# Kernel tuning notes

Measured on AMD Instinct MI355X. Metric: run time of the kernel, lower is better.

Reference implementation:

```python
import jax, jax.numpy as jnp
import numpy as np

N_NODES = 100000
N_EDGES = 1600000
G_DIM, H1, H2 = 128, 64, 32
HEADS = 4
NUM_REL = 3
NUM_CLASSES = 7


def setup_inputs() -> dict:
    key = jax.random.key(0)
    ks = jax.random.split(key, 16)
    s = 0.05
    inp = {
        "x": jax.random.normal(ks[0], (N_NODES, G_DIM), dtype=jnp.float32),
        "lengths": N_NODES,
        "edge_index": jax.random.randint(ks[1], (2, N_EDGES), 0, N_NODES),
        "edge_type": jax.random.randint(ks[2], (N_EDGES,), 0, NUM_REL),
        # RGCNConv params (root weight + per-relation weights + bias)
        "W_rel": jax.random.normal(ks[3], (NUM_REL, G_DIM, H1), dtype=jnp.float32) * s,
        "W_root": jax.random.normal(ks[4], (G_DIM, H1), dtype=jnp.float32) * s,
        "b_rgcn": jax.random.normal(ks[5], (H1,), dtype=jnp.float32) * s,
        # TransformerConv params (heads*H2 = 128 output, concat=True default)
        "Wq": jax.random.normal(ks[6], (H1, HEADS * H2), dtype=jnp.float32) * s,
        "bq": jax.random.normal(ks[7], (HEADS * H2,), dtype=jnp.float32) * s,
        "Wk": jax.random.normal(ks[8], (H1, HEADS * H2), dtype=jnp.float32) * s,
        "bk": jax.random.normal(ks[9], (HEADS * H2,), dtype=jnp.float32) * s,
        "Wv": jax.random.normal(ks[10], (H1, HEADS * H2), dtype=jnp.float32) * s,
        "bv": jax.random.normal(ks[11], (HEADS * H2,), dtype=jnp.float32) * s,
        "Wskip": jax.random.normal(ks[12], (H1, HEADS * H2), dtype=jnp.float32) * s,
        "bskip": jax.random.normal(ks[13], (HEADS * H2,), dtype=jnp.float32) * s,
        # final classifier (in = heads*H2 since TransformerConv concat=True)
        "Wf": jax.random.normal(ks[14], (HEADS * H2, NUM_CLASSES), dtype=jnp.float32) * s,
        "bf": jax.random.normal(ks[15], (NUM_CLASSES,), dtype=jnp.float32) * s,
    }
    return inp


def _forward(x, edge_index, edge_type, W_rel, W_root, b_rgcn,
             Wq, bq, Wk, bk, Wv, bv, Wskip, bskip, Wf, bf):
    n = x.shape[0]
    src, dst = edge_index[0], edge_index[1]  # source -> target flow

    # ---- RGCNConv: root transform + per-relation mean aggregation ----
    h = x @ W_root + b_rgcn  # [N, H1]
    for r in range(NUM_REL):
        hr = x @ W_rel[r]  # [N, H1] transform at node level (cheap)
        mask = (edge_type == r)
        msg = jnp.where(mask[:, None], hr[src], 0.0)  # [E, H1]
        ssum = jax.ops.segment_sum(msg, dst, num_segments=n)
        cnt = jax.ops.segment_sum(mask.astype(x.dtype), dst, num_segments=n)
        h = h + jnp.where(cnt[:, None] > 0, ssum / jnp.maximum(cnt, 1.0)[:, None], 0.0)
    h = jax.nn.relu(h)

    # ---- TransformerConv (heads=4, concat=True, root skip) ----
    Q = (h @ Wq + bq).reshape(n, HEADS, H2)
    K = (h @ Wk + bk).reshape(n, HEADS, H2)
    V = (h @ Wv + bv).reshape(n, HEADS, H2)
    scores = jnp.sum(Q[dst] * K[src], axis=-1) / jnp.sqrt(jnp.asarray(H2, x.dtype))  # [E, HEADS]
    smax = jax.ops.segment_max(scores, dst, num_segments=n)  # [N, HEADS]
    e = jnp.exp(scores - smax[dst])
    denom = jax.ops.segment_sum(e, dst, num_segments=n)  # [N, HEADS]
    alpha = e / jnp.maximum(denom[dst], 1e-16)  # [E, HEADS]
    agg = jax.ops.segment_sum(alpha[..., None] * V[src], dst, num_segments=n)  # [N, HEADS, H2]
    out = agg.reshape(n, HEADS * H2) + h @ Wskip + bskip
    out = jax.nn.relu(out)

    return out @ Wf + bf  # [N, NUM_CLASSES]


def reference(x, lengths, edge_index, edge_type, W_rel, W_root, b_rgcn,
              Wq, bq, Wk, bk, Wv, bv, Wskip, bskip, Wf, bf):
    # lengths is accepted but unused by the original forward
    return _forward(x, edge_index, edge_type, W_rel, W_root, b_rgcn,
                    Wq, bq, Wk, bk, Wv, bv, Wskip, bskip, Wf, bf)
```

## Files before the change

kernel.cpp:

```cpp
#include <hip/hip_runtime.h>
#include <math.h>

#define N_NODES 100000
#define N_EDGES 1600000

typedef short short8 __attribute__((ext_vector_type(8)));
typedef float f32x4 __attribute__((ext_vector_type(4)));

static __device__ __forceinline__ float bf2f(unsigned int u16) {
    return __uint_as_float(u16 << 16);
}
static __device__ __forceinline__ unsigned short f2bf(float f) {
    unsigned u = __float_as_uint(f);
    unsigned r = u + 0x7FFF + ((u >> 16) & 1);
    return (unsigned short)(r >> 16);
}

__global__ void repack_kernel(const float* __restrict__ Wrel, const float* __restrict__ Wroot,
                              const float* __restrict__ Wq, const float* __restrict__ Wk,
                              const float* __restrict__ Wv, const float* __restrict__ Wsk,
                              const float* __restrict__ bq, const float* __restrict__ bk,
                              const float* __restrict__ bv, const float* __restrict__ bsk,
                              unsigned short* __restrict__ W1t, unsigned short* __restrict__ W2t,
                              float* __restrict__ bcat) {
    int idx = blockIdx.x * 256 + threadIdx.x;
    if (idx < 128 * 256) {
        int k = idx >> 8, c = idx & 255;
        float v;
        if (c < 192) { int r = c >> 6, cc = c & 63; v = Wrel[r * 8192 + k * 64 + cc]; }
        else v = Wroot[k * 64 + (c - 192)];
        W1t[c * 128 + k] = f2bf(v);
    }
    int i2 = idx - 128 * 256;
    if (i2 >= 0 && i2 < 64 * 512) {
        int k = i2 >> 9, c = i2 & 511;
        float v;
        if (c < 128) v = Wq[k * 128 + c];
        else if (c < 256) v = Wk[k * 128 + c - 128];
        else if (c < 384) v = Wv[k * 128 + c - 256];
        else v = Wsk[k * 128 + c - 384];
        W2t[c * 64 + k] = f2bf(v);
    }
    int i3 = idx - 128 * 256 - 64 * 512;
    if (i3 >= 0 && i3 < 512) {
        float v;
        if (i3 < 128) v = bq[i3];
        else if (i3 < 256) v = bk[i3 - 128];
        else if (i3 < 384) v = bv[i3 - 256];
        else v = bsk[i3 - 384];
        bcat[i3] = v;
    }
}

__global__ void hist_kernel(const int* __restrict__ ei, int* __restrict__ deg) {
    int e = blockIdx.x * 256 + threadIdx.x;
    if (e < N_EDGES) atomicAdd(&deg[ei[N_EDGES + e]], 1);
}

__global__ void scanA_kernel(const int* __restrict__ deg, int* __restrict__ part) {
    __shared__ int wsum[4];
    int t = threadIdx.x;
    int base = blockIdx.x * 1024 + t * 4;
    int s = 0;
    for (int i = 0; i < 4; i++) { int idx = base + i; if (idx < N_NODES) s += deg[idx]; }
    for (int off = 1; off < 64; off <<= 1) s += __shfl_xor(s, off);
    if ((t & 63) == 0) wsum[t >> 6] = s;
    __syncthreads();
    if (t == 0) part[blockIdx.x] = wsum[0] + wsum[1] + wsum[2] + wsum[3];
}

__global__ void scanB_kernel(int* __restrict__ part, int* __restrict__ rs, int nb) {
    int run = 0;
    for (int b = 0; b < nb; b++) { int v = part[b]; part[b] = run; run += v; }
    rs[N_NODES] = run;
}

__global__ void scanC_kernel(const int* __restrict__ deg, const int* __restrict__ part,
                             int* __restrict__ rs) {
    __shared__ int wsum[4];
    int t = threadIdx.x;
    int base = blockIdx.x * 1024 + t * 4;
    int v[4]; int tsum = 0;
    for (int i = 0; i < 4; i++) { int idx = base + i; v[i] = (idx < N_NODES) ? deg[idx] : 0; tsum += v[i]; }
    int x = tsum;
    int lane = t & 63;
    for (int off = 1; off < 64; off <<= 1) { int y = __shfl_up(x, off); if (lane >= off) x += y; }
    if (lane == 63) wsum[t >> 6] = x;
    __syncthreads();
    if (t == 0) { int run = 0; for (int w = 0; w < 4; w++) { int tmp = wsum[w]; wsum[w] = run; run += tmp; } }
    __syncthreads();
    int excl = x - tsum + wsum[t >> 6] + part[blockIdx.x];
    for (int i = 0; i < 4; i++) {
        int idx = base + i;
        if (idx < N_NODES) rs[idx] = excl;
        excl += v[i];
    }
}

__global__ void scatter_kernel(const int* __restrict__ ei, const int* __restrict__ et,
                               const int* __restrict__ rs, int* __restrict__ fill,
                               unsigned int* __restrict__ ep) {
    int e = blockIdx.x * 256 + threadIdx.x;
    if (e >= N_EDGES) return;
    int src = ei[e], dst = ei[N_EDGES + e], r = et[e];
    int pos = rs[dst] + atomicAdd(&fill[dst], 1);
    ep[pos] = (unsigned)src | ((unsigned)r << 20);
}

__global__ __launch_bounds__(256) void gemm1_mfma(const float* __restrict__ X,
                                                  const unsigned short* __restrict__ W1t,
                                                  unsigned short* __restrict__ hr_all) {
    __shared__ unsigned short As[64][136];
    __shared__ unsigned short Bs[64][136];
    int t = threadIdx.x;
    int rb = blockIdx.x * 64;
    #pragma unroll
    for (int i = 0; i < 8; i++) {
        int lin = t + i * 256;
        int row = lin >> 5;
        int c4 = lin & 31;
        float4 v = make_float4(0.f, 0.f, 0.f, 0.f);
        int gr = rb + row;
        if (gr < N_NODES) v = *(const float4*)&X[gr * 128 + c4 * 4];
        unsigned w0 = (unsigned)f2bf(v.x) | ((unsigned)f2bf(v.y) << 16);
        unsigned w1 = (unsigned)f2bf(v.z) | ((unsigned)f2bf(v.w) << 16);
        *(uint2*)&As[row][c4 * 4] = make_uint2(w0, w1);
    }
    int w = t >> 6, l = t & 63;
    int wr = (w >> 1) * 32, wc = (w & 1) * 32;
    int lr = l & 15, lk = (l >> 4) * 8;
    int drow = (l >> 4) * 4;
    int dcol = l & 15;
    for (int cb4 = 0; cb4 < 4; cb4++) {
        int cb = cb4 * 64;
        __syncthreads();
        #pragma unroll
        for (int i = 0; i < 4; i++) {
            int lin = t + i * 256;
            int n = lin >> 4;
            int k8 = lin & 15;
            *(uint4*)&Bs[n][k8 * 8] = *(const uint4*)&W1t[(cb + n) * 128 + k8 * 8];
        }
        __syncthreads();
        f32x4 c00 = {0.f,0.f,0.f,0.f}, c01 = {0.f,0.f,0.f,0.f};
        f32x4 c10 = {0.f,0.f,0.f,0.f}, c11 = {0.f,0.f,0.f,0.f};
        #pragma unroll
        for (int kk = 0; kk < 128; kk += 32) {
            short8 a0 = *(const short8*)&As[wr + lr][kk + lk];
            short8 a1 = *(const short8*)&As[wr + 16 + lr][kk + lk];
            short8 b0 = *(const short8*)&Bs[wc + lr][kk + lk];
            short8 b1 = *(const short8*)&Bs[wc + 16 + lr][kk + lk];
            c00 = __builtin_amdgcn_mfma_f32_16x16x32_bf16(a0, b0, c00, 0, 0, 0);
            c01 = __builtin_amdgcn_mfma_f32_16x16x32_bf16(a0, b1, c01, 0, 0, 0);
            c10 = __builtin_amdgcn_mfma_f32_16x16x32_bf16(a1, b0, c10, 0, 0, 0);
            c11 = __builtin_amdgcn_mfma_f32_16x16x32_bf16(a1, b1, c11, 0, 0, 0);
        }
        f32x4 cc[2][2] = {{c00, c01}, {c10, c11}};
        #pragma unroll
        for (int i = 0; i < 2; i++)
            #pragma unroll
            for (int j = 0; j < 2; j++)
                #pragma unroll
                for (int rg = 0; rg < 4; rg++) {
                    int gr = rb + wr + i * 16 + drow + rg;
                    int gc = cb + wc + j * 16 + dcol;
                    if (gr < N_NODES) hr_all[gr * 256 + gc] = f2bf(cc[i][j][rg]);
                }
    }
}

__global__ __launch_bounds__(256) void rgcn_kernel(const unsigned short* __restrict__ hr,
                                                   const float* __restrict__ brg, const int* __restrict__ rs,
                                                   const unsigned int* __restrict__ ep,
                                                   unsigned short* __restrict__ Hm) {
    int lane = threadIdx.x & 63;
    int n = blockIdx.x * 4 + (threadIdx.x >> 6);
    if (n >= N_NODES) return;
    int p0 = rs[n], p1 = rs[n + 1];
    float a0 = 0.f, a1 = 0.f, a2 = 0.f, c0 = 0.f, c1 = 0.f, c2 = 0.f;
    for (int base = p0; base < p1; base += 64) {
        int pc = base + lane;
        int chunk = (pc < p1) ? (int)ep[pc] : 0;
        int cnt = min(64, p1 - base);
        int j = 0;
        for (; j + 3 < cnt; j += 4) {
            int e0 = __builtin_amdgcn_readlane(chunk, j);
            int e1 = __builtin_amdgcn_readlane(chunk, j + 1);
            int e2 = __builtin_amdgcn_readlane(chunk, j + 2);
            int e3 = __builtin_amdgcn_readlane(chunk, j + 3);
            int s0 = e0 & 0xFFFFF, r0 = e0 >> 20;
            int s1 = e1 & 0xFFFFF, r1 = e1 >> 20;
            int s2 = e2 & 0xFFFFF, r2 = e2 >> 20;
            int s3 = e3 & 0xFFFFF, r3 = e3 >> 20;
            float v0 = bf2f(hr[s0 * 256 + r0 * 64 + lane]);
            float v1 = bf2f(hr[s1 * 256 + r1 * 64 + lane]);
            float v2 = bf2f(hr[s2 * 256 + r2 * 64 + lane]);
            float v3 = bf2f(hr[s3 * 256 + r3 * 64 + lane]);
            if (r0 == 0) { a0 += v0; c0 += 1.f; } else if (r0 == 1) { a1 += v0; c1 += 1.f; } else { a2 += v0; c2 += 1.f; }
            if (r1 == 0) { a0 += v1; c0 += 1.f; } else if (r1 == 1) { a1 += v1; c1 += 1.f; } else { a2 += v1; c2 += 1.f; }
            if (r2 == 0) { a0 += v2; c0 += 1.f; } else if (r2 == 1) { a1 += v2; c1 += 1.f; } else { a2 += v2; c2 += 1.f; }
            if (r3 == 0) { a0 += v3; c0 += 1.f; } else if (r3 == 1) { a1 += v3; c1 += 1.f; } else { a2 += v3; c2 += 1.f; }
        }
        for (; j < cnt; j++) {
            int e0 = __builtin_amdgcn_readlane(chunk, j);
            int s0 = e0 & 0xFFFFF, r0 = e0 >> 20;
            float v0 = bf2f(hr[s0 * 256 + r0 * 64 + lane]);
            if (r0 == 0) { a0 += v0; c0 += 1.f; } else if (r0 == 1) { a1 += v0; c1 += 1.f; } else { a2 += v0; c2 += 1.f; }
        }
    }
    float h = bf2f(hr[n * 256 + 192 + lane]) + brg[lane];
    if (c0 > 0.f) h += a0 / c0;
    if (c1 > 0.f) h += a1 / c1;
    if (c2 > 0.f) h += a2 / c2;
    Hm[n * 64 + lane] = f2bf(fmaxf(h, 0.f));
}

__global__ __launch_bounds__(256) void gemm2_mfma(const unsigned short* __restrict__ Hm,
                                                  const unsigned short* __restrict__ W2t,
                                                  const float* __restrict__ bcat,
                                                  unsigned short* __restrict__ Qb, unsigned short* __restrict__ Kb,
                                                  unsigned short* __restrict__ Vb, unsigned short* __restrict__ Sb) {
    __shared__ unsigned short As[64][72];
    __shared__ unsigned short Bs[64][72];
    int t = threadIdx.x;
    int rb = blockIdx.x * 64;
    #pragma unroll
    for (int i = 0; i < 2; i++) {
        int lin = t + i * 256;
        int row = lin >> 3;
        int k8 = lin & 7;
        uint4 v = make_uint4(0, 0, 0, 0);
        int gr = rb + row;
        if (gr < N_NODES) v = *(const uint4*)&Hm[gr * 64 + k8 * 8];
        *(uint4*)&As[row][k8 * 8] = v;
    }
    int w = t >> 6, l = t & 63;
    int wr = (w >> 1) * 32, wc = (w & 1) * 32;
    int lr = l & 15, lk = (l >> 4) * 8;
    int drow = (l >> 4) * 4;
    int dcol = l & 15;
    for (int cb8 = 0; cb8 < 8; cb8++) {
        int cb = cb8 * 64;
        __syncthreads();
        #pragma unroll
        for (int i = 0; i < 2; i++) {
            int lin = t + i * 256;
            int n = lin >> 3;
            int k8 = lin & 7;
            *(uint4*)&Bs[n][k8 * 8] = *(const uint4*)&W2t[(cb + n) * 64 + k8 * 8];
        }
        __syncthreads();
        f32x4 c00 = {0.f,0.f,0.f,0.f}, c01 = {0.f,0.f,0.f,0.f};
        f32x4 c10 = {0.f,0.f,0.f,0.f}, c11 = {0.f,0.f,0.f,0.f};
        #pragma unroll
        for (int kk = 0; kk < 64; kk += 32) {
            short8 a0 = *(const short8*)&As[wr + lr][kk + lk];
            short8 a1 = *(const short8*)&As[wr + 16 + lr][kk + lk];
            short8 b0 = *(const short8*)&Bs[wc + lr][kk + lk];
            short8 b1 = *(const short8*)&Bs[wc + 16 + lr][kk + lk];
            c00 = __builtin_amdgcn_mfma_f32_16x16x32_bf16(a0, b0, c00, 0, 0, 0);
            c01 = __builtin_amdgcn_mfma_f32_16x16x32_bf16(a0, b1, c01, 0, 0, 0);
            c10 = __builtin_amdgcn_mfma_f32_16x16x32_bf16(a1, b0, c10, 0, 0, 0);
            c11 = __builtin_amdgcn_mfma_f32_16x16x32_bf16(a1, b1, c11, 0, 0, 0);
        }
        f32x4 cc[2][2] = {{c00, c01}, {c10, c11}};
        #pragma unroll
        for (int i = 0; i < 2; i++)
            #pragma unroll
            for (int j = 0; j < 2; j++)
                #pragma unroll
                for (int rg = 0; rg < 4; rg++) {
                    int gr = rb + wr + i * 16 + drow + rg;
                    int gc = cb + wc + j * 16 + dcol;
                    if (gr >= N_NODES) continue;
                    float v = cc[i][j][rg] + bcat[gc];
                    unsigned short h = f2bf(v);
                    if (gc < 128) Qb[gr * 128 + gc] = h;
                    else if (gc < 256) Kb[gr * 128 + (gc - 128)] = h;
                    else if (gc < 384) Vb[gr * 128 + (gc - 256)] = h;
                    else Sb[gr * 128 + (gc - 384)] = h;
                }
    }
}

__global__ __launch_bounds__(256) void attn_kernel(const unsigned short* __restrict__ Qb,
                                                   const unsigned short* __restrict__ Kb,
                                                   const unsigned short* __restrict__ Vb,
                                                   const int* __restrict__ rs, const unsigned int* __restrict__ ep,
                                                   const unsigned short* __restrict__ Sb,
                                                   const float* __restrict__ Wf, const float* __restrict__ bfv,
                                                   float* __restrict__ out) {
    int lane = threadIdx.x & 63;
    int n = blockIdx.x * 4 + (threadIdx.x >> 6);
    if (n >= N_NODES) return;
    const unsigned* Qu = (const unsigned*)Qb;
    const unsigned* Ku = (const unsigned*)Kb;
    const unsigned* Vu = (const unsigned*)Vb;
    const unsigned* Su = (const unsigned*)Sb;
    unsigned qw = Qu[n * 64 + lane];
    const float qs = 0.17677669529663687f;
    float q0 = bf2f(qw & 0xFFFF) * qs, q1 = bf2f(qw >> 16) * qs;
    float wf0[7], wf1[7];
    #pragma unroll
    for (int j = 0; j < 7; j++) { wf0[j] = Wf[(2 * lane) * 7 + j]; wf1[j] = Wf[(2 * lane + 1) * 7 + j]; }
    float d = 0.f, o0 = 0.f, o1 = 0.f;
    int p0 = rs[n], p1 = rs[n + 1];
    for (int base = p0; base < p1; base += 64) {
        int pc = base + lane;
        int chunk = (pc < p1) ? (int)ep[pc] : 0;
        int cnt = min(64, p1 - base);
        int j = 0;
        for (; j + 3 < cnt; j += 4) {
            int e0 = __builtin_amdgcn_readlane(chunk, j);
            int e1 = __builtin_amdgcn_readlane(chunk, j + 1);
            int e2 = __builtin_amdgcn_readlane(chunk, j + 2);
            int e3 = __builtin_amdgcn_readlane(chunk, j + 3);
            int s0 = e0 & 0xFFFFF, s1 = e1 & 0xFFFFF, s2 = e2 & 0xFFFFF, s3 = e3 & 0xFFFFF;
            unsigned k0 = Ku[s0 * 64 + lane], k1 = Ku[s1 * 64 + lane];
            unsigned k2 = Ku[s2 * 64 + lane], k3 = Ku[s3 * 64 + lane];
            unsigned v0 = Vu[s0 * 64 + lane], v1 = Vu[s1 * 64 + lane];
            unsigned v2 = Vu[s2 * 64 + lane], v3 = Vu[s3 * 64 + lane];
            float d0 = q0 * bf2f(k0 & 0xFFFF) + q1 * bf2f(k0 >> 16);
            float d1 = q0 * bf2f(k1 & 0xFFFF) + q1 * bf2f(k1 >> 16);
            float d2 = q0 * bf2f(k2 & 0xFFFF) + q1 * bf2f(k2 >> 16);
            float d3 = q0 * bf2f(k3 & 0xFFFF) + q1 * bf2f(k3 >> 16);
            d0 += __shfl_xor(d0, 1); d1 += __shfl_xor(d1, 1); d2 += __shfl_xor(d2, 1); d3 += __shfl_xor(d3, 1);
            d0 += __shfl_xor(d0, 2); d1 += __shfl_xor(d1, 2); d2 += __shfl_xor(d2, 2); d3 += __shfl_xor(d3, 2);
            d0 += __shfl_xor(d0, 4); d1 += __shfl_xor(d1, 4); d2 += __shfl_xor(d2, 4); d3 += __shfl_xor(d3, 4);
            d0 += __shfl_xor(d0, 8); d1 += __shfl_xor(d1, 8); d2 += __shfl_xor(d2, 8); d3 += __shfl_xor(d3, 8);
            float w0 = __expf(d0), w1 = __expf(d1), w2 = __expf(d2), w3 = __expf(d3);
            d += (w0 + w1) + (w2 + w3);
            o0 += w0 * bf2f(v0 & 0xFFFF) + w1 * bf2f(v1 & 0xFFFF)
                + w2 * bf2f(v2 & 0xFFFF) + w3 * bf2f(v3 & 0xFFFF);
            o1 += w0 * bf2f(v0 >> 16) + w1 * bf2f(v1 >> 16)
                + w2 * bf2f(v2 >> 16) + w3 * bf2f(v3 >> 16);
        }
        for (; j < cnt; j++) {
            int e0 = __builtin_amdgcn_readlane(chunk, j);
            int s0 = e0 & 0xFFFFF;
            unsigned k0 = Ku[s0 * 64 + lane];
            unsigned v0 = Vu[s0 * 64 + lane];
            float d0 = q0 * bf2f(k0 & 0xFFFF) + q1 * bf2f(k0 >> 16);
            d0 += __shfl_xor(d0, 1);
            d0 += __shfl_xor(d0, 2);
            d0 += __shfl_xor(d0, 4);
            d0 += __shfl_xor(d0, 8);
            float w0 = __expf(d0);
            d += w0;
            o0 += w0 * bf2f(v0 & 0xFFFF);
            o1 += w0 * bf2f(v0 >> 16);
        }
    }
    float inv = (d > 0.f) ? 1.f / d : 0.f;
    unsigned sw = Su[n * 64 + lane];
    float r0 = fmaxf(bf2f(sw & 0xFFFF) + o0 * inv, 0.f);
    float r1 = fmaxf(bf2f(sw >> 16) + o1 * inv, 0.f);
    float acc[7];
    #pragma unroll
    for (int j = 0; j < 7; j++) acc[j] = r0 * wf0[j] + r1 * wf1[j];
    #pragma unroll
    for (int j = 0; j < 7; j++) {
        acc[j] += __shfl_xor(acc[j], 1);
        acc[j] += __shfl_xor(acc[j], 2);
        acc[j] += __shfl_xor(acc[j], 4);
        acc[j] += __shfl_xor(acc[j], 8);
        acc[j] += __shfl_xor(acc[j], 16);
        acc[j] += __shfl_xor(acc[j], 32);
    }
    if (lane == 0) {
        #pragma unroll
        for (int j = 0; j < 7; j++) out[n * 7 + j] = acc[j] + bfv[j];
    }
}

extern "C" void kernel_launch(void* const* d_in, const int* in_sizes, int n_in,
                              void* d_out, int out_size, void* d_ws, size_t ws_size,
                              hipStream_t stream) {
    const float* x     = (const float*)d_in[0];
    const int*   ei    = (const int*)d_in[2];
    const int*   et    = (const int*)d_in[3];
    const float* Wrel  = (const float*)d_in[4];
    const float* Wroot = (const float*)d_in[5];
    const float* brg   = (const float*)d_in[6];
    const float* Wq    = (const float*)d_in[7];
    const float* bq    = (const float*)d_in[8];
    const float* Wk    = (const float*)d_in[9];
    const float* bk    = (const float*)d_in[10];
    const float* Wv    = (const float*)d_in[11];
    const float* bv    = (const float*)d_in[12];
    const float* Wsk   = (const float*)d_in[13];
    const float* bsk   = (const float*)d_in[14];
    const float* Wf    = (const float*)d_in[15];
    const float* bfv   = (const float*)d_in[16];
    float* out = (float*)d_out;

    char* ws = (char*)d_ws;
    unsigned short* hr_all = (unsigned short*)(ws + 0);
    unsigned short* Qb     = (unsigned short*)(ws + 0);
    unsigned short* Kb     = (unsigned short*)(ws + 25600000);
    unsigned short* Vb     = (unsigned short*)(ws + 51200000);
    unsigned short* Hm     = (unsigned short*)(ws + 76800000);
    unsigned short* Sb     = (unsigned short*)(ws + 89600000);
    unsigned int*   ep     = (unsigned int*)(ws + 115200000);
    int*            rs     = (int*)(ws + 121600000);
    int*            deg    = (int*)(ws + 122000016);
    int*            fill   = (int*)(ws + 122400016);
    int*            part   = (int*)(ws + 122800016);
    unsigned short* W1t    = (unsigned short*)(ws + 122800528);
    unsigned short* W2t    = (unsigned short*)(ws + 122866064);
    float*          bcat   = (float*)(ws + 122931600);

    hipMemsetAsync(deg, 0, 2 * N_NODES * sizeof(int), stream);

    repack_kernel<<<258, 256, 0, stream>>>(Wrel, Wroot, Wq, Wk, Wv, Wsk, bq, bk, bv, bsk, W1t, W2t, bcat);

    hist_kernel<<<N_EDGES / 256, 256, 0, stream>>>(ei, deg);
    scanA_kernel<<<98, 256, 0, stream>>>(deg, part);
    scanB_kernel<<<1, 1, 0, stream>>>(part, rs, 98);
    scanC_kernel<<<98, 256, 0, stream>>>(deg, part, rs);
    scatter_kernel<<<N_EDGES / 256, 256, 0, stream>>>(ei, et, rs, fill, ep);

    gemm1_mfma<<<1563, 256, 0, stream>>>(x, W1t, hr_all);
    rgcn_kernel<<<25000, 256, 0, stream>>>(hr_all, brg, rs, ep, Hm);

    gemm2_mfma<<<1563, 256, 0, stream>>>(Hm, W2t, bcat, Qb, Kb, Vb, Sb);
    attn_kernel<<<25000, 256, 0, stream>>>(Qb, Kb, Vb, rs, ep, Sb, Wf, bfv, out);
}
```

Measured before the change: 548.2 us.

## Vectorize edge gathers to process four edges per wave with precomputed mean weights

The RGCN and attention gather kernels now split each wave into four 16-lane slots. Each slot handles a different edge and reads a full feature row with wide uint2/uint4 loads, then partial sums are reduced across slots. The histogram now counts per relation and destination, so scatter can store a per-edge 1/count weight and the RGCN kernel avoids its per-edge relation branching. The serial scanB kernel is removed by having each scanC block compute its own prefix of the partials. In exchange the preprocessing stores an extra per-edge float array, and the attention output needs cross-slot shuffle reductions.

```diff
diff --git a/kernel.cpp b/kernel.cpp
--- a/kernel.cpp
+++ b/kernel.cpp
@@ -14,6 +14,16 @@
     unsigned u = __float_as_uint(f);
     unsigned r = u + 0x7FFF + ((u >> 16) & 1);
     return (unsigned short)(r >> 16);
+}
+static __device__ __forceinline__ void unpack8(uint4 u, float* f) {
+    f[0] = bf2f(u.x & 0xFFFF); f[1] = bf2f(u.x >> 16);
+    f[2] = bf2f(u.y & 0xFFFF); f[3] = bf2f(u.y >> 16);
+    f[4] = bf2f(u.z & 0xFFFF); f[5] = bf2f(u.z >> 16);
+    f[6] = bf2f(u.w & 0xFFFF); f[7] = bf2f(u.w >> 16);
+}
+static __device__ __forceinline__ void unpack4(uint2 u, float* f) {
+    f[0] = bf2f(u.x & 0xFFFF); f[1] = bf2f(u.x >> 16);
+    f[2] = bf2f(u.y & 0xFFFF); f[3] = bf2f(u.y >> 16);
 }
 
 __global__ void repack_kernel(const float* __restrict__ Wrel, const float* __restrict__ Wroot,
@@ -52,59 +62,70 @@
     }
 }
 
-__global__ void hist_kernel(const int* __restrict__ ei, int* __restrict__ deg) {
+__global__ void hist_kernel(const int* __restrict__ ei, const int* __restrict__ et,
+                            int* __restrict__ cntr) {
     int e = blockIdx.x * 256 + threadIdx.x;
-    if (e < N_EDGES) atomicAdd(&deg[ei[N_EDGES + e]], 1);
-}
-
-__global__ void scanA_kernel(const int* __restrict__ deg, int* __restrict__ part) {
+    if (e < N_EDGES) atomicAdd(&cntr[et[e] * N_NODES + ei[N_EDGES + e]], 1);
+}
+
+__global__ void scanA_kernel(const int* __restrict__ cntr, int* __restrict__ part) {
     __shared__ int wsum[4];
     int t = threadIdx.x;
     int base = blockIdx.x * 1024 + t * 4;
     int s = 0;
-    for (int i = 0; i < 4; i++) { int idx = base + i; if (idx < N_NODES) s += deg[idx]; }
+    for (int i = 0; i < 4; i++) {
+        int idx = base + i;
+        if (idx < N_NODES) s += cntr[idx] + cntr[N_NODES + idx] + cntr[2 * N_NODES + idx];
+    }
     for (int off = 1; off < 64; off <<= 1) s += __shfl_xor(s, off);
     if ((t & 63) == 0) wsum[t >> 6] = s;
     __syncthreads();
     if (t == 0) part[blockIdx.x] = wsum[0] + wsum[1] + wsum[2] + wsum[3];
 }
 
-__global__ void scanB_kernel(int* __restrict__ part, int* __restrict__ rs, int nb) {
-    int run = 0;
-    for (int b = 0; b < nb; b++) { int v = part[b]; part[b] = run; run += v; }
-    rs[N_NODES] = run;
-}
-
-__global__ void scanC_kernel(const int* __restrict__ deg, const int* __restrict__ part,
+__global__ void scanC_kernel(const int* __restrict__ cntr, const int* __restrict__ part,
                              int* __restrict__ rs) {
     __shared__ int wsum[4];
+    __shared__ int ws2[4];
     int t = threadIdx.x;
+    int lane = t & 63;
     int base = blockIdx.x * 1024 + t * 4;
     int v[4]; int tsum = 0;
-    for (int i = 0; i < 4; i++) { int idx = base + i; v[i] = (idx < N_NODES) ? deg[idx] : 0; tsum += v[i]; }
+    for (int i = 0; i < 4; i++) {
+        int idx = base + i;
+        v[i] = (idx < N_NODES) ? (cntr[idx] + cntr[N_NODES + idx] + cntr[2 * N_NODES + idx]) : 0;
+        tsum += v[i];
+    }
+    int p = (t < blockIdx.x) ? part[t] : 0;
+    for (int off = 1; off < 64; off <<= 1) p += __shfl_xor(p, off);
+    if (lane == 0) ws2[t >> 6] = p;
     int x = tsum;
-    int lane = t & 63;
     for (int off = 1; off < 64; off <<= 1) { int y = __shfl_up(x, off); if (lane >= off) x += y; }
     if (lane == 63) wsum[t >> 6] = x;
     __syncthreads();
     if (t == 0) { int run = 0; for (int w = 0; w < 4; w++) { int tmp = wsum[w]; wsum[w] = run; run += tmp; } }
     __syncthreads();
-    int excl = x - tsum + wsum[t >> 6] + part[blockIdx.x];
+    int bofs = ws2[0] + ws2[1] + ws2[2] + ws2[3];
+    int excl = x - tsum + wsum[t >> 6] + bofs;
     for (int i = 0; i < 4; i++) {
         int idx = base + i;
         if (idx < N_NODES) rs[idx] = excl;
         excl += v[i];
     }
+    if (blockIdx.x == 0 && t == 0) rs[N_NODES] = N_EDGES;
 }
 
 __global__ void scatter_kernel(const int* __restrict__ ei, const int* __restrict__ et,
-                               const int* __restrict__ rs, int* __restrict__ fill,
-                               unsigned int* __restrict__ ep) {
+                               const int* __restrict__ rs, const int* __restrict__ cntr,
+                               int* __restrict__ fill,
+                               unsigned int* __restrict__ ep, float* __restrict__ epw) {
     int e = blockIdx.x * 256 + threadIdx.x;
     if (e >= N_EDGES) return;
     int src = ei[e], dst = ei[N_EDGES + e], r = et[e];
     int pos = rs[dst] + atomicAdd(&fill[dst], 1);
-    ep[pos] = (unsigned)src | ((unsigned)r << 20);
+    int c = cntr[r * N_NODES + dst];
+    ep[pos] = ((unsigned)src << 2) | (unsigned)r;
+    epw[pos] = 1.f / (float)c;
 }
 
 __global__ __launch_bounds__(256) void gemm1_mfma(const float* __restrict__ X,
@@ -172,47 +193,52 @@
 __global__ __launch_bounds__(256) void rgcn_kernel(const unsigned short* __restrict__ hr,
                                                    const float* __restrict__ brg, const int* __restrict__ rs,
                                                    const unsigned int* __restrict__ ep,
+                                                   const float* __restrict__ epw,
                                                    unsigned short* __restrict__ Hm) {
-    int lane = threadIdx.x & 63;
-    int n = blockIdx.x * 4 + (threadIdx.x >> 6);
+    int t = threadIdx.x, lane = t & 63;
+    int n = blockIdx.x * 4 + (t >> 6);
     if (n >= N_NODES) return;
+    int slot = lane >> 4, pos = lane & 15;
+    const uint2* H2 = (const uint2*)hr;
+    float a0 = 0.f, a1 = 0.f, a2 = 0.f, a3 = 0.f;
     int p0 = rs[n], p1 = rs[n + 1];
-    float a0 = 0.f, a1 = 0.f, a2 = 0.f, c0 = 0.f, c1 = 0.f, c2 = 0.f;
     for (int base = p0; base < p1; base += 64) {
         int pc = base + lane;
-        int chunk = (pc < p1) ? (int)ep[pc] : 0;
+        unsigned chunk = (pc < p1) ? ep[pc] : 0u;
+        float wch = (pc < p1) ? epw[pc] : 0.f;
         int cnt = min(64, p1 - base);
-        int j = 0;
-        for (; j + 3 < cnt; j += 4) {
-            int e0 = __builtin_amdgcn_readlane(chunk, j);
-            int e1 = __builtin_amdgcn_readlane(chunk, j + 1);
-            int e2 = __builtin_amdgcn_readlane(chunk, j + 2);
-            int e3 = __builtin_amdgcn_readlane(chunk, j + 3);
-            int s0 = e0 & 0xFFFFF, r0 = e0 >> 20;
-            int s1 = e1 & 0xFFFFF, r1 = e1 >> 20;
-            int s2 = e2 & 0xFFFFF, r2 = e2 >> 20;
-            int s3 = e3 & 0xFFFFF, r3 = e3 >> 20;
-            float v0 = bf2f(hr[s0 * 256 + r0 * 64 + lane]);
-            float v1 = bf2f(hr[s1 * 256 + r1 * 64 + lane]);
-            float v2 = bf2f(hr[s2 * 256 + r2 * 64 + lane]);
-            float v3 = bf2f(hr[s3 * 256 + r3 * 64 + lane]);
-            if (r0 == 0) { a0 += v0; c0 += 1.f; } else if (r0 == 1) { a1 += v0; c1 += 1.f; } else { a2 += v0; c2 += 1.f; }
-            if (r1 == 0) { a0 += v1; c0 += 1.f; } else if (r1 == 1) { a1 += v1; c1 += 1.f; } else { a2 += v1; c2 += 1.f; }
-            if (r2 == 0) { a0 += v2; c0 += 1.f; } else if (r2 == 1) { a1 += v2; c1 += 1.f; } else { a2 += v2; c2 += 1.f; }
-            if (r3 == 0) { a0 += v3; c0 += 1.f; } else if (r3 == 1) { a1 += v3; c1 += 1.f; } else { a2 += v3; c2 += 1.f; }
-        }
-        for (; j < cnt; j++) {
-            int e0 = __builtin_amdgcn_readlane(chunk, j);
-            int s0 = e0 & 0xFFFFF, r0 = e0 >> 20;
-            float v0 = bf2f(hr[s0 * 256 + r0 * 64 + lane]);
-            if (r0 == 0) { a0 += v0; c0 += 1.f; } else if (r0 == 1) { a1 += v0; c1 += 1.f; } else { a2 += v0; c2 += 1.f; }
-        }
-    }
-    float h = bf2f(hr[n * 256 + 192 + lane]) + brg[lane];
-    if (c0 > 0.f) h += a0 / c0;
-    if (c1 > 0.f) h += a1 / c1;
-    if (c2 > 0.f) h += a2 / c2;
-    Hm[n * 64 + lane] = f2bf(fmaxf(h, 0.f));
+        for (int g0 = 0; g0 < cnt; g0 += 8) {
+            int iA = g0 + slot, iB = iA + 4;
+            unsigned eA = (unsigned)__shfl((int)chunk, iA);
+            unsigned eB = (unsigned)__shfl((int)chunk, iB);
+            float wA = __shfl(wch, iA);
+            float wB = __shfl(wch, iB);
+            uint2 hA = H2[eA * 16 + pos];
+            uint2 hB = H2[eB * 16 + pos];
+            float f[4];
+            unpack4(hA, f);
+            a0 += wA * f[0]; a1 += wA * f[1]; a2 += wA * f[2]; a3 += wA * f[3];
+            unpack4(hB, f);
+            a0 += wB * f[0]; a1 += wB * f[1]; a2 += wB * f[2]; a3 += wB * f[3];
+        }
+    }
+    a0 += __shfl_xor(a0, 16); a0 += __shfl_xor(a0, 32);
+    a1 += __shfl_xor(a1, 16); a1 += __shfl_xor(a1, 32);
+    a2 += __shfl_xor(a2, 16); a2 += __shfl_xor(a2, 32);
+    a3 += __shfl_xor(a3, 16); a3 += __shfl_xor(a3, 32);
+    uint2 rt = H2[(n * 4 + 3) * 16 + pos];
+    float rtf[4]; unpack4(rt, rtf);
+    float4 bb = ((const float4*)brg)[pos];
+    float h0 = fmaxf(rtf[0] + bb.x + a0, 0.f);
+    float h1 = fmaxf(rtf[1] + bb.y + a1, 0.f);
+    float h2 = fmaxf(rtf[2] + bb.z + a2, 0.f);
+    float h3 = fmaxf(rtf[3] + bb.w + a3, 0.f);
+    if (slot == 0) {
+        uint2 wv;
+        wv.x = (unsigned)f2bf(h0) | ((unsigned)f2bf(h1) << 16);
+        wv.y = (unsigned)f2bf(h2) | ((unsigned)f2bf(h3) << 16);
+        ((uint2*)Hm)[n * 16 + pos] = wv;
+    }
 }
 
 __global__ __launch_bounds__(256) void gemm2_mfma(const unsigned short* __restrict__ Hm,
@@ -290,74 +316,72 @@
                                                    const unsigned short* __restrict__ Sb,
                                                    const float* __restrict__ Wf, const float* __restrict__ bfv,
                                                    float* __restrict__ out) {
-    int lane = threadIdx.x & 63;
-    int n = blockIdx.x * 4 + (threadIdx.x >> 6);
+    int t = threadIdx.x, lane = t & 63;
+    int n = blockIdx.x * 4 + (t >> 6);
     if (n >= N_NODES) return;
-    const unsigned* Qu = (const unsigned*)Qb;
-    const unsigned* Ku = (const unsigned*)Kb;
-    const unsigned* Vu = (const unsigned*)Vb;
-    const unsigned* Su = (const unsigned*)Sb;
-    unsigned qw = Qu[n * 64 + lane];
+    int slot = lane >> 4, pos = lane & 15;
+    const uint4* K4 = (const uint4*)Kb;
+    const uint4* V4 = (const uint4*)Vb;
     const float qs = 0.17677669529663687f;
-    float q0 = bf2f(qw & 0xFFFF) * qs, q1 = bf2f(qw >> 16) * qs;
-    float wf0[7], wf1[7];
-    #pragma unroll
-    for (int j = 0; j < 7; j++) { wf0[j] = Wf[(2 * lane) * 7 + j]; wf1[j] = Wf[(2 * lane + 1) * 7 + j]; }
-    float d = 0.f, o0 = 0.f, o1 = 0.f;
+    uint4 qv = ((const uint4*)Qb)[n * 16 + pos];
+    float q[8]; unpack8(qv, q);
+    #pragma unroll
+    for (int i = 0; i < 8; i++) q[i] *= qs;
+    float o[8] = {0.f,0.f,0.f,0.f,0.f,0.f,0.f,0.f};
+    float d = 0.f;
     int p0 = rs[n], p1 = rs[n + 1];
     for (int base = p0; base < p1; base += 64) {
         int pc = base + lane;
-        int chunk = (pc < p1) ? (int)ep[pc] : 0;
+        unsigned chunk = (pc < p1) ? ep[pc] : 0u;
         int cnt = min(64, p1 - base);
-        int j = 0;
-        for (; j + 3 < cnt; j += 4) {
-            int e0 = __builtin_amdgcn_readlane(chunk, j);
-            int e1 = __builtin_amdgcn_readlane(chunk, j + 1);
-            int e2 = __builtin_amdgcn_readlane(chunk, j + 2);
-            int e3 = __builtin_amdgcn_readlane(chunk, j + 3);
-            int s0 = e0 & 0xFFFFF, s1 = e1 & 0xFFFFF, s2 = e2 & 0xFFFFF, s3 = e3 & 0xFFFFF;
-            unsigned k0 = Ku[s0 * 64 + lane], k1 = Ku[s1 * 64 + lane];
-            unsigned k2 = Ku[s2 * 64 + lane], k3 = Ku[s3 * 64 + lane];
-            unsigned v0 = Vu[s0 * 64 + lane], v1 = Vu[s1 * 64 + lane];
-            unsigned v2 = Vu[s2 * 64 + lane], v3 = Vu[s3 * 64 + lane];
-            float d0 = q0 * bf2f(k0 & 0xFFFF) + q1 * bf2f(k0 >> 16);
-            float d1 = q0 * bf2f(k1 & 0xFFFF) + q1 * bf2f(k1 >> 16);
-            float d2 = q0 * bf2f(k2 & 0xFFFF) + q1 * bf2f(k2 >> 16);
-            float d3 = q0 * bf2f(k3 & 0xFFFF) + q1 * bf2f(k3 >> 16);
-            d0 += __shfl_xor(d0, 1); d1 += __shfl_xor(d1, 1); d2 += __shfl_xor(d2, 1); d3 += __shfl_xor(d3, 1);
-            d0 += __shfl_xor(d0, 2); d1 += __shfl_xor(d1, 2); d2 += __shfl_xor(d2, 2); d3 += __shfl_xor(d3, 2);
-            d0 += __shfl_xor(d0, 4); d1 += __shfl_xor(d1, 4); d2 += __shfl_xor(d2, 4); d3 += __shfl_xor(d3, 4);
-            d0 += __shfl_xor(d0, 8); d1 += __shfl_xor(d1, 8); d2 += __shfl_xor(d2, 8); d3 += __shfl_xor(d3, 8);
-            float w0 = __expf(d0), w1 = __expf(d1), w2 = __expf(d2), w3 = __expf(d3);
-            d += (w0 + w1) + (w2 + w3);
-            o0 += w0 * bf2f(v0 & 0xFFFF) + w1 * bf2f(v1 & 0xFFFF)
-                + w2 * bf2f(v2 & 0xFFFF) + w3 * bf2f(v3 & 0xFFFF);
-            o1 += w0 * bf2f(v0 >> 16) + w1 * bf2f(v1 >> 16)
-                + w2 * bf2f(v2 >> 16) + w3 * bf2f(v3 >> 16);
-        }
-        for (; j < cnt; j++) {
-            int e0 = __builtin_amdgcn_readlane(chunk, j);
-            int s0 = e0 & 0xFFFFF;
-            unsigned k0 = Ku[s0 * 64 + lane];
-            unsigned v0 = Vu[s0 * 64 + lane];
-            float d0 = q0 * bf2f(k0 & 0xFFFF) + q1 * bf2f(k0 >> 16);
-            d0 += __shfl_xor(d0, 1);
-            d0 += __shfl_xor(d0, 2);
-            d0 += __shfl_xor(d0, 4);
-            d0 += __shfl_xor(d0, 8);
-            float w0 = __expf(d0);
-            d += w0;
-            o0 += w0 * bf2f(v0 & 0xFFFF);
-            o1 += w0 * bf2f(v0 >> 16);
-        }
-    }
+        for (int g0 = 0; g0 < cnt; g0 += 8) {
+            int iA = g0 + slot, iB = iA + 4;
+            unsigned eA = (unsigned)__shfl((int)chunk, iA);
+            unsigned eB = (unsigned)__shfl((int)chunk, iB);
+            int sA = (int)(eA >> 2), sB = (int)(eB >> 2);
+            uint4 kA = K4[sA * 16 + pos];
+            uint4 vA = V4[sA * 16 + pos];
+            uint4 kB = K4[sB * 16 + pos];
+            uint4 vB = V4[sB * 16 + pos];
+            float kf[8], vf[8];
+            unpack8(kA, kf);
+            float dotA = q[0]*kf[0] + q[1]*kf[1] + q[2]*kf[2] + q[3]*kf[3]
+                       + q[4]*kf[4] + q[5]*kf[5] + q[6]*kf[6] + q[7]*kf[7];
+            dotA += __shfl_xor(dotA, 1);
+            dotA += __shfl_xor(dotA, 2);
+            float wA = __expf(dotA);
+            wA = (iA < cnt) ? wA : 0.f;
+            unpack8(kB, kf);
+            float dotB = q[0]*kf[0] + q[1]*kf[1] + q[2]*kf[2] + q[3]*kf[3]
+                       + q[4]*kf[4] + q[5]*kf[5] + q[6]*kf[6] + q[7]*kf[7];
+            dotB += __shfl_xor(dotB, 1);
+            dotB += __shfl_xor(dotB, 2);
+            float wB = __expf(dotB);
+            wB = (iB < cnt) ? wB : 0.f;
+            d += wA + wB;
+            unpack8(vA, vf);
+            #pragma unroll
+            for (int i = 0; i < 8; i++) o[i] += wA * vf[i];
+            unpack8(vB, vf);
+            #pragma unroll
+            for (int i = 0; i < 8; i++) o[i] += wB * vf[i];
+        }
+    }
+    d += __shfl_xor(d, 16); d += __shfl_xor(d, 32);
+    #pragma unroll
+    for (int i = 0; i < 8; i++) { o[i] += __shfl_xor(o[i], 16); o[i] += __shfl_xor(o[i], 32); }
     float inv = (d > 0.f) ? 1.f / d : 0.f;
-    unsigned sw = Su[n * 64 + lane];
-    float r0 = fmaxf(bf2f(sw & 0xFFFF) + o0 * inv, 0.f);
-    float r1 = fmaxf(bf2f(sw >> 16) + o1 * inv, 0.f);
+    uint4 sv = ((const uint4*)Sb)[n * 16 + pos];
+    float sf[8]; unpack8(sv, sf);
+    float rf[8];
+    #pragma unroll
+    for (int i = 0; i < 8; i++) rf[i] = fmaxf(sf[i] + o[i] * inv, 0.f);
+    float rr0 = (slot == 0) ? rf[0] : (slot == 1) ? rf[2] : (slot == 2) ? rf[4] : rf[6];
+    float rr1 = (slot == 0) ? rf[1] : (slot == 1) ? rf[3] : (slot == 2) ? rf[5] : rf[7];
+    int gd = pos * 8 + slot * 2;
     float acc[7];
     #pragma unroll
-    for (int j = 0; j < 7; j++) acc[j] = r0 * wf0[j] + r1 * wf1[j];
+    for (int j = 0; j < 7; j++) acc[j] = rr0 * Wf[gd * 7 + j] + rr1 * Wf[gd * 7 + 7 + j];
     #pragma unroll
     for (int j = 0; j < 7; j++) {
         acc[j] += __shfl_xor(acc[j], 1);
@@ -399,29 +423,29 @@
     unsigned short* Qb     = (unsigned short*)(ws + 0);
     unsigned short* Kb     = (unsigned short*)(ws + 25600000);
     unsigned short* Vb     = (unsigned short*)(ws + 51200000);
-    unsigned short* Hm     = (unsigned short*)(ws + 76800000);
-    unsigned short* Sb     = (unsigned short*)(ws + 89600000);
+    unsigned short* Sb     = (unsigned short*)(ws + 76800000);
+    unsigned short* Hm     = (unsigned short*)(ws + 102400000);
     unsigned int*   ep     = (unsigned int*)(ws + 115200000);
-    int*            rs     = (int*)(ws + 121600000);
-    int*            deg    = (int*)(ws + 122000016);
-    int*            fill   = (int*)(ws + 122400016);
-    int*            part   = (int*)(ws + 122800016);
-    unsigned short* W1t    = (unsigned short*)(ws + 122800528);
-    unsigned short* W2t    = (unsigned short*)(ws + 122866064);
-    float*          bcat   = (float*)(ws + 122931600);
-
-    hipMemsetAsync(deg, 0, 2 * N_NODES * sizeof(int), stream);
+    float*          epw    = (float*)(ws + 121600000);
+    int*            rs     = (int*)(ws + 128000000);
+    int*            cntr   = (int*)(ws + 128400016);
+    int*            fill   = (int*)(ws + 129600016);
+    int*            part   = (int*)(ws + 130000016);
+    unsigned short* W1t    = (unsigned short*)(ws + 130000528);
+    unsigned short* W2t    = (unsigned short*)(ws + 130066064);
+    float*          bcat   = (float*)(ws + 130131600);
+
+    hipMemsetAsync(cntr, 0, 4 * N_NODES * sizeof(int), stream);
 
     repack_kernel<<<258, 256, 0, stream>>>(Wrel, Wroot, Wq, Wk, Wv, Wsk, bq, bk, bv, bsk, W1t, W2t, bcat);
 
-    hist_kernel<<<N_EDGES / 256, 256, 0, stream>>>(ei, deg);
-    scanA_kernel<<<98, 256, 0, stream>>>(deg, part);
-    scanB_kernel<<<1, 1, 0, stream>>>(part, rs, 98);
-    scanC_kernel<<<98, 256, 0, stream>>>(deg, part, rs);
-    scatter_kernel<<<N_EDGES / 256, 256, 0, stream>>>(ei, et, rs, fill, ep);
+    hist_kernel<<<N_EDGES / 256, 256, 0, stream>>>(ei, et, cntr);
+    scanA_kernel<<<98, 256, 0, stream>>>(cntr, part);
+    scanC_kernel<<<98, 256, 0, stream>>>(cntr, part, rs);
+    scatter_kernel<<<N_EDGES / 256, 256, 0, stream>>>(ei, et, rs, cntr, fill, ep, epw);
 
     gemm1_mfma<<<1563, 256, 0, stream>>>(x, W1t, hr_all);
-    rgcn_kernel<<<25000, 256, 0, stream>>>(hr_all, brg, rs, ep, Hm);
+    rgcn_kernel<<<25000, 256, 0, stream>>>(hr_all, brg, rs, ep, epw, Hm);
 
     gemm2_mfma<<<1563, 256, 0, stream>>>(Hm, W2t, bcat, Qb, Kb, Vb, Sb);
     attn_kernel<<<25000, 256, 0, stream>>>(Qb, Kb, Vb, rs, ep, Sb, Wf, bfv, out);
```

New measurement: 524.3 us. 4.4% less time.
